# Performance work log

Hardware: AMD Instinct MI355X
Metric: run time of the kernel (lower is better)

Reference implementation:

```python
import jax, jax.numpy as jnp
from jax import lax
import numpy as np

B, L, C = 512, 2048, 64
START, STOP = 62, 63
NEG_INF = -10000.0


def setup_inputs() -> dict:
    key = jax.random.key(0)
    k1, k2, k3 = jax.random.split(key, 3)
    emissions = jax.random.normal(k1, (B, L, C), dtype=jnp.float32)
    transitions = jax.random.normal(k2, (C, C), dtype=jnp.float32)
    # forbid transitioning INTO start and OUT OF stop, as in __init__
    transitions = transitions.at[:, START].set(NEG_INF)
    transitions = transitions.at[STOP, :].set(NEG_INF)
    tags = jax.random.randint(k3, (B, L), 0, START, dtype=jnp.int32)  # real tags only
    mask = jnp.ones((B, L), dtype=jnp.float32)
    return {"emissions": emissions, "transitions": transitions, "mask": mask, "tags": tags}


def _crf_nll(emissions, transitions, mask, tags):
    # ----- gold path scores (vectorized _compute_scores) -----
    first_tags = tags[:, 0]
    e0 = jnp.take_along_axis(emissions[:, 0], first_tags[:, None], axis=1)[:, 0]
    scores = e0 + transitions[START, first_tags]
    # steps 1..L-1
    e = jnp.take_along_axis(emissions[:, 1:], tags[:, 1:, None], axis=2)[:, :, 0]  # (B, L-1)
    t = transitions[tags[:, :-1], tags[:, 1:]]                                      # (B, L-1)
    scores = scores + jnp.sum((e + t) * mask[:, 1:], axis=1)
    last_idx = mask.sum(axis=1).astype(jnp.int32) - 1
    last_tags = jnp.take_along_axis(tags, last_idx[:, None], axis=1)[:, 0]
    scores = scores + transitions[last_tags, STOP]

    # ----- log partition (forward algorithm as a single scan) -----
    alpha0 = emissions[:, 0] + transitions[START][None, :]  # (B, C)

    def step(alpha, xs):
        em_t, m_t = xs  # (B, C), (B,)
        # logsumexp over previous tag axis; emission added after (constant over that axis)
        new = jax.nn.logsumexp(alpha[:, :, None] + transitions[None, :, :], axis=1) + em_t
        alpha = jnp.where(m_t[:, None] > 0, new, alpha)
        return alpha, None

    ems = jnp.swapaxes(emissions[:, 1:], 0, 1)  # (L-1, B, C)
    ms = mask[:, 1:].T                           # (L-1, B)
    alpha, _ = lax.scan(step, alpha0, (ems, ms))
    partition = jax.nn.logsumexp(alpha + transitions[:, STOP][None, :], axis=1)  # (B,)

    return jnp.mean(partition - scores)


def reference(emissions, transitions, mask, tags):
    return _crf_nll(emissions, transitions, mask, tags)
```

## Files before the change

### kernel.cpp

```cpp
#include <hip/hip_runtime.h>

#define NB 512
#define NL 2048
#define NC 64
#define START_TAG 62
#define STOP_TAG 63

static __device__ __forceinline__ float2 f2(float x, float y) {
    float2 r; r.x = x; r.y = y; return r;
}

__global__ __launch_bounds__(64) void crf_fused(
    const float* __restrict__ em, const float* __restrict__ T,
    const float* __restrict__ mask, const int* __restrict__ tags,
    float* __restrict__ out)
{
    const int bid  = blockIdx.x;
    const int lane = threadIdx.x;
    const float LOG2E = 1.4426950408889634f;
    const float LN2   = 0.6931471805599453f;

    if (bid < NB) {
        const int b  = bid;
        const int h  = lane >> 5;
        const int pl = lane ^ 32;

        __shared__ alignas(16) float pbuf[2][NC];

        float2 colA2[16], colB2[16];
        #pragma unroll
        for (int k = 0; k < 16; ++k) {
            const int r0 = 32 * h + 2 * k;
            const int r1 = r0 + 1;
            colA2[k].x = exp2f(LOG2E * T[r0 * NC + lane]);
            colA2[k].y = exp2f(LOG2E * T[r1 * NC + lane]);
            colB2[k].x = exp2f(LOG2E * T[r0 * NC + pl]);
            colB2[k].y = exp2f(LOG2E * T[r1 * NC + pl]);
        }
        const float tstop = exp2f(LOG2E * T[lane * NC + STOP_TAG]);

        const float* emrow = em + (size_t)b * (NL * NC);
        const float* mrow  = mask + (size_t)b * NL;

        float pj = exp2f(LOG2E * (emrow[lane] + T[START_TAG * NC + lane]));
        int   E  = 0;

        auto step = [&](int parity, bool renorm, float em_c, float m_c) {
            if (renorm) {
                unsigned rb = (unsigned)__builtin_amdgcn_readfirstlane((int)__float_as_uint(pj));
                int ex = (int)((rb >> 23) & 0xFFu) - 127;
                pj = ldexpf(pj, -ex);
                E += ex;
            }
            float expem = exp2f(LOG2E * em_c);

            pbuf[parity][lane] = pj;
            asm volatile("s_waitcnt lgkmcnt(0)" ::: "memory");

            const float4* pb4 = (const float4*)(&pbuf[parity][0]) + 8 * h;
            float2 a0 = f2(0.f, 0.f), a1 = f2(0.f, 0.f);
            float2 b0 = f2(0.f, 0.f), b1 = f2(0.f, 0.f);
            #pragma unroll
            for (int ii = 0; ii < 8; ii += 2) {
                float4 q = pb4[ii];
                a0 += f2(q.x, q.y) * colA2[2 * ii + 0];
                b0 += f2(q.x, q.y) * colB2[2 * ii + 0];
                a0 += f2(q.z, q.w) * colA2[2 * ii + 1];
                b0 += f2(q.z, q.w) * colB2[2 * ii + 1];
                float4 r = pb4[ii + 1];
                a1 += f2(r.x, r.y) * colA2[2 * ii + 2];
                b1 += f2(r.x, r.y) * colB2[2 * ii + 2];
                a1 += f2(r.z, r.w) * colA2[2 * ii + 3];
                b1 += f2(r.z, r.w) * colB2[2 * ii + 3];
            }
            float2 sa2 = a0 + a1;
            float2 sb2 = b0 + b1;
            float sa = sa2.x + sa2.y;
            float sb = sb2.x + sb2.y;
            float sbp = __shfl_xor(sb, 32);
            float pnew = (sa + sbp) * expem;
            pj = (m_c > 0.0f) ? pnew : pj;
        };

        float emv[8]; float mv[8];
        #pragma unroll
        for (int k = 0; k < 8; ++k) {
            emv[k] = emrow[(1 + k) * NC + lane];
            mv[k]  = mrow[1 + k];
        }

        int tb = 1;
        for (; tb + 7 <= NL - 1; tb += 8) {
            #pragma unroll
            for (int k = 0; k < 8; ++k) {
                float em_c = emv[k], m_c = mv[k];
                int tn = tb + k + 8;
                if (tn > NL - 1) tn = NL - 1;
                emv[k] = emrow[tn * NC + lane];
                mv[k]  = mrow[tn];
                step(k & 1, (k & 3) == 0, em_c, m_c);
            }
        }
        #pragma unroll
        for (int k = 0; k < 7; ++k) step(k & 1, (k & 3) == 0, emv[k], mv[k]);

        float tsum = pj * tstop;
        #pragma unroll
        for (int off = 32; off > 0; off >>= 1) tsum += __shfl_xor(tsum, off);
        if (lane == 0) {
            float partition = LN2 * ((float)E + log2f(tsum));
            atomicAdd(out, partition * (1.0f / (float)NB));
        }
    } else {
        const int b = bid - NB;
        const float* emb = em + (size_t)b * (NL * NC);
        const float* mb  = mask + (size_t)b * NL;
        const int*   tg_ = tags + (size_t)b * NL;

        float s = 0.0f, msum = 0.0f;
        for (int it = 0; it < NL / 64; ++it) {
            int t = it * 64 + lane;
            float m = mb[t];
            msum += m;
            int tg = tg_[t];
            if (t == 0) {
                s += emb[tg] + T[START_TAG * NC + tg];
            } else {
                int pt = tg_[t - 1];
                s += m * (emb[t * NC + tg] + T[pt * NC + tg]);
            }
        }
        #pragma unroll
        for (int off = 32; off > 0; off >>= 1) {
            s    += __shfl_xor(s, off);
            msum += __shfl_xor(msum, off);
        }
        if (lane == 0) {
            int last = (int)(msum + 0.5f) - 1;
            int ltag = tg_[last];
            s += T[ltag * NC + STOP_TAG];
            atomicAdd(out, -s * (1.0f / (float)NB));
        }
    }
}

extern "C" void kernel_launch(void* const* d_in, const int* in_sizes, int n_in,
                              void* d_out, int out_size, void* d_ws, size_t ws_size,
                              hipStream_t stream) {
    const float* em   = (const float*)d_in[0];
    const float* T    = (const float*)d_in[1];
    const float* mask = (const float*)d_in[2];
    const int*   tags = (const int*)d_in[3];
    float* out = (float*)d_out;

    hipMemsetAsync(out, 0, sizeof(float), stream);
    crf_fused<<<dim3(2 * NB), dim3(64), 0, stream>>>(em, T, mask, tags, out);
}
```

Before: 827.0 us.

## Replace LDS broadcast of alpha with DPP/shuffle butterfly gather in CRF forward

Each forward-algorithm step now exchanges the 64 alpha values with one cross-half shuffle plus a tree of DPP row-shift moves that gathers 32 values per lane, instead of writing to LDS and reading them back as float4s. The transition exponentials are permuted to match the gather order, using a staged LDS copy of T. The exp of the emissions is hoisted into the prefetch so it leaves the serial chain, and renormalisation folds the scale into the emission factor rather than rescaling alpha. This aims to cut LDS round-trip latency on the sequential critical path, at the cost of extra VALU/DPP instructions and scalar FMAs in place of packed float2 math.

Result: faster. 784.9 us (-5.1%).

```diff
diff --git a/kernel.cpp b/kernel.cpp
--- a/kernel.cpp
+++ b/kernel.cpp
@@ -6,8 +6,21 @@
 #define START_TAG 62
 #define STOP_TAG 63
 
-static __device__ __forceinline__ float2 f2(float x, float y) {
-    float2 r; r.x = x; r.y = y; return r;
+static __device__ __forceinline__ void gather32(unsigned x, unsigned v[32]) {
+    v[0] = x;
+    v[1] = (unsigned)__shfl_xor((int)x, 16, 64);
+    #pragma unroll
+    for (int r = 0; r < 2; ++r)
+        v[2 + r] = (unsigned)__builtin_amdgcn_update_dpp(0, (int)v[r], 0x128, 0xF, 0xF, true);
+    #pragma unroll
+    for (int r = 0; r < 4; ++r)
+        v[4 + r] = (unsigned)__builtin_amdgcn_update_dpp(0, (int)v[r], 0x124, 0xF, 0xF, true);
+    #pragma unroll
+    for (int r = 0; r < 8; ++r)
+        v[8 + r] = (unsigned)__builtin_amdgcn_update_dpp(0, (int)v[r], 0x122, 0xF, 0xF, true);
+    #pragma unroll
+    for (int r = 0; r < 16; ++r)
+        v[16 + r] = (unsigned)__builtin_amdgcn_update_dpp(0, (int)v[r], 0x121, 0xF, 0xF, true);
 }
 
 __global__ __launch_bounds__(64) void crf_fused(
@@ -22,91 +35,86 @@
 
     if (bid < NB) {
         const int b  = bid;
-        const int h  = lane >> 5;
         const int pl = lane ^ 32;
 
-        __shared__ alignas(16) float pbuf[2][NC];
+        __shared__ float Traw[NC * NC];
+        #pragma unroll
+        for (int i = 0; i < NC; ++i) Traw[i * NC + lane] = T[i * NC + lane];
+        __syncthreads();
 
-        float2 colA2[16], colB2[16];
+        unsigned idx[32];
+        gather32((unsigned)lane, idx);
+
+        float cA[32], cB[32];
         #pragma unroll
-        for (int k = 0; k < 16; ++k) {
-            const int r0 = 32 * h + 2 * k;
-            const int r1 = r0 + 1;
-            colA2[k].x = exp2f(LOG2E * T[r0 * NC + lane]);
-            colA2[k].y = exp2f(LOG2E * T[r1 * NC + lane]);
-            colB2[k].x = exp2f(LOG2E * T[r0 * NC + pl]);
-            colB2[k].y = exp2f(LOG2E * T[r1 * NC + pl]);
+        for (int r = 0; r < 32; ++r) {
+            int i = (int)idx[r];
+            cA[r] = exp2f(LOG2E * Traw[i * NC + lane]);
+            cB[r] = exp2f(LOG2E * Traw[i * NC + pl]);
         }
-        const float tstop = exp2f(LOG2E * T[lane * NC + STOP_TAG]);
+        const float tstop = exp2f(LOG2E * Traw[lane * NC + STOP_TAG]);
 
         const float* emrow = em + (size_t)b * (NL * NC);
         const float* mrow  = mask + (size_t)b * NL;
 
-        float pj = exp2f(LOG2E * (emrow[lane] + T[START_TAG * NC + lane]));
+        float pj = exp2f(LOG2E * (emrow[lane] + Traw[START_TAG * NC + lane]));
         int   E  = 0;
 
-        auto step = [&](int parity, bool renorm, float em_c, float m_c) {
+        auto step = [&](bool renorm, float expem, float m_c) {
+            int ex = 0;
             if (renorm) {
                 unsigned rb = (unsigned)__builtin_amdgcn_readfirstlane((int)__float_as_uint(pj));
-                int ex = (int)((rb >> 23) & 0xFFu) - 127;
-                pj = ldexpf(pj, -ex);
-                E += ex;
+                unsigned e8 = (rb >> 23) & 0xFFu;
+                if (e8 != 0u) { ex = (int)e8 - 127; E += ex; }
             }
-            float expem = exp2f(LOG2E * em_c);
+            unsigned v[32];
+            gather32(__float_as_uint(pj), v);
 
-            pbuf[parity][lane] = pj;
-            asm volatile("s_waitcnt lgkmcnt(0)" ::: "memory");
-
-            const float4* pb4 = (const float4*)(&pbuf[parity][0]) + 8 * h;
-            float2 a0 = f2(0.f, 0.f), a1 = f2(0.f, 0.f);
-            float2 b0 = f2(0.f, 0.f), b1 = f2(0.f, 0.f);
+            float a0 = 0.f, a1 = 0.f, a2 = 0.f, a3 = 0.f;
+            float b0 = 0.f, b1 = 0.f, b2 = 0.f, b3 = 0.f;
             #pragma unroll
-            for (int ii = 0; ii < 8; ii += 2) {
-                float4 q = pb4[ii];
-                a0 += f2(q.x, q.y) * colA2[2 * ii + 0];
-                b0 += f2(q.x, q.y) * colB2[2 * ii + 0];
-                a0 += f2(q.z, q.w) * colA2[2 * ii + 1];
-                b0 += f2(q.z, q.w) * colB2[2 * ii + 1];
-                float4 r = pb4[ii + 1];
-                a1 += f2(r.x, r.y) * colA2[2 * ii + 2];
-                b1 += f2(r.x, r.y) * colB2[2 * ii + 2];
-                a1 += f2(r.z, r.w) * colA2[2 * ii + 3];
-                b1 += f2(r.z, r.w) * colB2[2 * ii + 3];
+            for (int r = 0; r < 32; r += 4) {
+                a0 = fmaf(__uint_as_float(v[r + 0]), cA[r + 0], a0);
+                a1 = fmaf(__uint_as_float(v[r + 1]), cA[r + 1], a1);
+                a2 = fmaf(__uint_as_float(v[r + 2]), cA[r + 2], a2);
+                a3 = fmaf(__uint_as_float(v[r + 3]), cA[r + 3], a3);
+                b0 = fmaf(__uint_as_float(v[r + 0]), cB[r + 0], b0);
+                b1 = fmaf(__uint_as_float(v[r + 1]), cB[r + 1], b1);
+                b2 = fmaf(__uint_as_float(v[r + 2]), cB[r + 2], b2);
+                b3 = fmaf(__uint_as_float(v[r + 3]), cB[r + 3], b3);
             }
-            float2 sa2 = a0 + a1;
-            float2 sb2 = b0 + b1;
-            float sa = sa2.x + sa2.y;
-            float sb = sb2.x + sb2.y;
-            float sbp = __shfl_xor(sb, 32);
-            float pnew = (sa + sbp) * expem;
+            float sa = (a0 + a1) + (a2 + a3);
+            float sb = (b0 + b1) + (b2 + b3);
+            float sbp = __shfl_xor(sb, 32, 64);
+            float pnew = (sa + sbp) * ldexpf(expem, -ex);
             pj = (m_c > 0.0f) ? pnew : pj;
         };
 
-        float emv[8]; float mv[8];
+        float expemv[8]; float mv[8];
         #pragma unroll
         for (int k = 0; k < 8; ++k) {
-            emv[k] = emrow[(1 + k) * NC + lane];
-            mv[k]  = mrow[1 + k];
+            expemv[k] = exp2f(LOG2E * emrow[(1 + k) * NC + lane]);
+            mv[k]     = mrow[1 + k];
         }
 
         int tb = 1;
         for (; tb + 7 <= NL - 1; tb += 8) {
             #pragma unroll
             for (int k = 0; k < 8; ++k) {
-                float em_c = emv[k], m_c = mv[k];
+                float ev = expemv[k], m_c = mv[k];
                 int tn = tb + k + 8;
                 if (tn > NL - 1) tn = NL - 1;
-                emv[k] = emrow[tn * NC + lane];
-                mv[k]  = mrow[tn];
-                step(k & 1, (k & 3) == 0, em_c, m_c);
+                expemv[k] = exp2f(LOG2E * emrow[tn * NC + lane]);
+                mv[k]     = mrow[tn];
+                step((k & 3) == 0, ev, m_c);
             }
         }
         #pragma unroll
-        for (int k = 0; k < 7; ++k) step(k & 1, (k & 3) == 0, emv[k], mv[k]);
+        for (int k = 0; k < 7; ++k) step((k & 3) == 0, expemv[k], mv[k]);
 
         float tsum = pj * tstop;
         #pragma unroll
-        for (int off = 32; off > 0; off >>= 1) tsum += __shfl_xor(tsum, off);
+        for (int off = 32; off > 0; off >>= 1) tsum += __shfl_xor(tsum, off, 64);
         if (lane == 0) {
             float partition = LN2 * ((float)E + log2f(tsum));
             atomicAdd(out, partition * (1.0f / (float)NB));
@@ -132,8 +140,8 @@
         }
         #pragma unroll
         for (int off = 32; off > 0; off >>= 1) {
-            s    += __shfl_xor(s, off);
-            msum += __shfl_xor(msum, off);
+            s    += __shfl_xor(s, off, 64);
+            msum += __shfl_xor(msum, off, 64);
         }
         if (lane == 0) {
             int last = (int)(msum + 0.5f) - 1;
```
